# Kernel tuning notes

Measured on AMD Instinct MI355X. Metric: run time of the kernel, lower is better.

## Reference

```python
import jax, jax.numpy as jnp
import numpy as np

N = 50000      # nodes
E = 800000     # edges
IN_DIM = 256
H = 128
OUT_DIM = 64
DEPTH = 3
NEG_SLOPE = 0.2  # DGL GATConv default leaky_relu slope


def setup_inputs() -> dict:
    key = jax.random.key(0)
    ks = jax.random.split(key, 20)
    def nrm(k, shape, fan_in):
        return jax.random.normal(k, shape, jnp.float32) / jnp.sqrt(jnp.float32(fan_in))
    x = jax.random.normal(ks[0], (N, IN_DIM), jnp.float32)
    src = jax.random.randint(ks[1], (E,), 0, N, jnp.int32)
    dst = jax.random.randint(ks[2], (E,), 0, N, jnp.int32)
    # weights stored as [in, out] (y = x @ W + b)
    inp = dict(
        x=x, src=src, dst=dst,
        wx_W=nrm(ks[3], (IN_DIM, H), IN_DIM), wx_b=jnp.zeros((H,), jnp.float32),
        gat_W=nrm(ks[4], (DEPTH, H, H), H), gat_b=jnp.zeros((DEPTH, H), jnp.float32),
        attn_l=nrm(ks[5], (DEPTH, H), H), attn_r=nrm(ks[6], (DEPTH, H), H),
        ig_W=nrm(ks[7], (DEPTH, 2 * H, H), 2 * H), ig_b=jnp.zeros((DEPTH, H), jnp.float32),
        fg_W=nrm(ks[8], (DEPTH, 2 * H, H), 2 * H), fg_b=jnp.zeros((DEPTH, H), jnp.float32),
        og_W=nrm(ks[9], (DEPTH, 2 * H, H), 2 * H), og_b=jnp.zeros((DEPTH, H), jnp.float32),
        st_W=nrm(ks[10], (DEPTH, 2 * H, H), 2 * H), st_b=jnp.zeros((DEPTH, H), jnp.float32),
        out_W=nrm(ks[11], (H, OUT_DIM), H), out_b=jnp.zeros((OUT_DIM,), jnp.float32),
    )
    return inp


def _breadth(h, W, b, a_l, a_r, src, dst):
    """DGL GATConv with 1 head + tanh activation; mean over heads is identity."""
    z = h @ W                                  # [N, H]
    el = z @ a_l                               # [N]
    er = z @ a_r                               # [N]
    e = jax.nn.leaky_relu(el[src] + er[dst], NEG_SLOPE)   # [E]
    # edge softmax over incoming edges of each dst node
    emax = jax.ops.segment_max(e, dst, num_segments=N)    # [N]
    emax = jnp.where(jnp.isfinite(emax), emax, 0.0)       # guard isolated nodes
    ex = jnp.exp(e - emax[dst])                            # [E]
    denom = jax.ops.segment_sum(ex, dst, num_segments=N)   # [N]
    alpha = ex / jnp.maximum(denom, 1e-16)[dst]             # [E]
    agg = jax.ops.segment_sum(alpha[:, None] * z[src], dst, num_segments=N)  # [N, H]
    return jnp.tanh(agg + b)


def reference(x, src, dst, wx_W, wx_b, gat_W, gat_b, attn_l, attn_r,
              ig_W, ig_b, fg_W, fg_b, og_W, og_b, st_W, st_b, out_W, out_b):
    h0 = x @ wx_W + wx_b                       # [N, H]
    h = h0
    collector = []
    for i in range(DEPTH):
        h = _breadth(h, gat_W[i], gat_b[i], attn_l[i], attn_r[i], src, dst)
        collector.append(h)
    mu = h0
    c = jnp.zeros_like(mu)
    for i in range(DEPTH):
        hm = jnp.concatenate([collector[i], mu], axis=1)   # [N, 2H]
        ig = jax.nn.sigmoid(hm @ ig_W[i] + ig_b[i])
        fg = jax.nn.sigmoid(hm @ fg_W[i] + fg_b[i])
        og = jax.nn.sigmoid(hm @ og_W[i] + og_b[i])
        c_tilde = jnp.tanh(hm @ st_W[i] + st_b[i])
        c = fg * c + ig * c_tilde
        mu = og * jnp.tanh(c)
    return jax.nn.relu(mu @ out_W + out_b)     # [N, OUT_DIM]
```

## Files before the change

kernel.cpp:

```cpp
#include <hip/hip_runtime.h>
#include <math.h>
#include <type_traits>

#define NN 50000
#define EE 800000
#define IN_D 256
#define HH 128
#define OUT_D 64
#define DEPTH 3
#define BK 512
#define NBK 98

typedef unsigned short u16;
typedef __bf16  bf16x8 __attribute__((ext_vector_type(8)));
typedef short   short8 __attribute__((ext_vector_type(8)));
typedef float   f32x4  __attribute__((ext_vector_type(4)));

__device__ __forceinline__ u16 f2b(float f){
    unsigned u = __float_as_uint(f);
    u += 0x7fff + ((u>>16)&1);
    return (u16)(u>>16);
}
__device__ __forceinline__ float b2f(u16 h){ return __uint_as_float(((unsigned)h)<<16); }

#define LOG2E 1.4426950408889634f
#if __has_builtin(__builtin_amdgcn_exp2f)
__device__ __forceinline__ float fexp2(float x){ return __builtin_amdgcn_exp2f(x); }
#else
__device__ __forceinline__ float fexp2(float x){ return exp2f(x); }
#endif
#if __has_builtin(__builtin_amdgcn_rcpf)
__device__ __forceinline__ float frcp(float x){ return __builtin_amdgcn_rcpf(x); }
#else
__device__ __forceinline__ float frcp(float x){ return 1.f/x; }
#endif
__device__ __forceinline__ float sigm(float x){ return frcp(1.f + fexp2(-x*LOG2E)); }
__device__ __forceinline__ float ftanh(float x){
    float ax = fabsf(x);
    float u = fexp2(ax * (-2.f*LOG2E));
    float r = (1.f - u) * frcp(1.f + u);
    return copysignf(r, x);
}

enum { EPI_BF=0, EPI_RELU=1, EPI_ZEL=2 };

template<int EPI, int WAVES, int CT, int K, typename TA>
__global__ __launch_bounds__(WAVES*64, 4) void rgemm_k(
    const TA* __restrict__ A1,
    const u16* __restrict__ Bp,
    const float* __restrict__ b1, const float* __restrict__ b2,
    void* __restrict__ Out, float* __restrict__ aux1, float* __restrict__ aux2,
    int Nrows)
{
    constexpr int TH = WAVES*64;
    constexpr int KS = K/32;
    constexpr int M  = WAVES*CT*16;
    __shared__ u16 As[64*K];
    __shared__ float elp[(EPI==EPI_ZEL)?64*WAVES:1];
    __shared__ float erp[(EPI==EPI_ZEL)?64*WAVES:1];

    const int tid = threadIdx.x;
    const int rb  = blockIdx.x*64;

    constexpr int CHUNKS = 64*K/(TH*8);
    #pragma unroll
    for (int c = 0; c < CHUNKS; ++c) {
        int cidx = tid + c*TH;
        int row = cidx & 63, kseg = cidx >> 6;
        int grow = rb + row; if (grow >= Nrows) grow = Nrows-1;
        short8 v;
        if constexpr (std::is_same<TA,float>::value) {
            const float* p = (const float*)A1 + (size_t)grow*K + kseg*8;
            float4 x0 = *(const float4*)p;
            float4 x1 = *(const float4*)(p+4);
            v[0]=(short)f2b(x0.x); v[1]=(short)f2b(x0.y); v[2]=(short)f2b(x0.z); v[3]=(short)f2b(x0.w);
            v[4]=(short)f2b(x1.x); v[5]=(short)f2b(x1.y); v[6]=(short)f2b(x1.z); v[7]=(short)f2b(x1.w);
        } else {
            v = *(const short8*)((const u16*)A1 + (size_t)grow*K + kseg*8);
        }
        int byte = ((row>>4)*KS + (kseg>>2))*1024 + ((kseg&3)*16 + (row&15))*16;
        *(short8*)((char*)As + byte) = v;
    }
    __syncthreads();

    const int lane = tid & 63, w = tid >> 6;
    const int ml = lane & 15, ksel = lane >> 4;
    f32x4 acc[4][CT] = {};
    #pragma unroll
    for (int ks = 0; ks < KS; ++ks) {
        bf16x8 a[4];
        #pragma unroll
        for (int rt = 0; rt < 4; ++rt)
            a[rt] = *(const bf16x8*)((const char*)As + (rt*KS + ks)*1024 + lane*16);
        #pragma unroll
        for (int j = 0; j < CT; ++j) {
            int ctg = j*WAVES + w;
            bf16x8 b = *(const bf16x8*)(Bp + (((size_t)(ctg*KS + ks))<<9) + lane*8);
            #pragma unroll
            for (int rt = 0; rt < 4; ++rt)
                acc[rt][j] = __builtin_amdgcn_mfma_f32_16x16x32_bf16(a[rt], b, acc[rt][j], 0,0,0);
        }
    }

    if constexpr (EPI==EPI_BF || EPI==EPI_RELU) {
        #pragma unroll
        for (int rt = 0; rt < 4; ++rt)
        #pragma unroll
        for (int r = 0; r < 4; ++r) {
            int row = rb + rt*16 + ksel*4 + r;
            if (row >= Nrows) continue;
            #pragma unroll
            for (int j = 0; j < CT; ++j) {
                int gc = (j*WAVES + w)*16 + ml;
                float vv = acc[rt][j][r] + b1[gc];
                if (EPI==EPI_BF) ((u16*)Out)[(size_t)row*M + gc]   = f2b(vv);
                else             ((float*)Out)[(size_t)row*M + gc] = fmaxf(vv, 0.f);
            }
        }
    } else {
        float pel[4][4] = {}, per[4][4] = {};
        #pragma unroll
        for (int j = 0; j < CT; ++j) {
            int gc = (j*WAVES + w)*16 + ml;
            float alc = b1[gc], arc = b2[gc];
            #pragma unroll
            for (int rt = 0; rt < 4; ++rt)
            #pragma unroll
            for (int r = 0; r < 4; ++r) {
                int row = rb + rt*16 + ksel*4 + r;
                float vv = acc[rt][j][r];
                if (row < Nrows) ((u16*)Out)[(size_t)row*HH + gc] = f2b(vv);
                pel[rt][r] = fmaf(vv, alc, pel[rt][r]);
                per[rt][r] = fmaf(vv, arc, per[rt][r]);
            }
        }
        #pragma unroll
        for (int msk = 1; msk < 16; msk <<= 1)
            #pragma unroll
            for (int rt = 0; rt < 4; ++rt)
            #pragma unroll
            for (int r = 0; r < 4; ++r) {
                pel[rt][r] += __shfl_xor(pel[rt][r], msk);
                per[rt][r] += __shfl_xor(per[rt][r], msk);
            }
        if (ml == 0) {
            #pragma unroll
            for (int rt = 0; rt < 4; ++rt)
            #pragma unroll
            for (int r = 0; r < 4; ++r) {
                int lr = rt*16 + ksel*4 + r;
                elp[lr*WAVES + w] = pel[rt][r];
                erp[lr*WAVES + w] = per[rt][r];
            }
        }
        __syncthreads();
        if (tid < 64) {
            int row = rb + tid;
            if (row < Nrows) {
                float s1 = 0.f, s2 = 0.f;
                #pragma unroll
                for (int wv = 0; wv < WAVES; ++wv) { s1 += elp[tid*WAVES+wv]; s2 += erp[tid*WAVES+wv]; }
                aux1[row] = s1; aux2[row] = s2;
            }
        }
    }
}

__global__ __launch_bounds__(512, 3) void depth_k(
    const u16* __restrict__ coll0, const u16* __restrict__ coll1, const u16* __restrict__ coll2,
    const u16* __restrict__ mu0,
    const u16* __restrict__ gateP, const u16* __restrict__ outP,
    const float* __restrict__ igb, const float* __restrict__ stb,
    const float* __restrict__ fgb, const float* __restrict__ ogb,
    const float* __restrict__ outb, float* __restrict__ Out,
    int Nrows)
{
    __shared__ u16 As[64*HH];
    __shared__ u16 Ms[64*HH];
    const int tid = threadIdx.x;
    const int rb  = blockIdx.x*64;
    const int lane = tid & 63, w = tid >> 6;
    const int ml = lane & 15, ksel = lane >> 4;
    const int gcg = w*16 + ml;

    const int c0 = tid, c1 = tid + 512;
    const int row0 = c0 & 63, kg0 = c0 >> 6;
    const int row1 = c1 & 63, kg1 = c1 >> 6;
    int gr0 = rb + row0; if (gr0 >= Nrows) gr0 = Nrows-1;
    int gr1 = rb + row1; if (gr1 >= Nrows) gr1 = Nrows-1;
    const size_t off0 = (size_t)gr0*HH + kg0*8, off1 = (size_t)gr1*HH + kg1*8;
    const int dst0 = ((row0>>4)*4 + (kg0>>2))*1024 + ((kg0&3)*16 + (row0&15))*16;
    const int dst1 = ((row1>>4)*4 + (kg1>>2))*1024 + ((kg1&3)*16 + (row1&15))*16;

    *(short8*)((char*)Ms + dst0) = *(const short8*)(mu0 + off0);
    *(short8*)((char*)Ms + dst1) = *(const short8*)(mu0 + off1);
    short8 pf0 = *(const short8*)(coll0 + off0);
    short8 pf1 = *(const short8*)(coll0 + off1);

    float cc[4][4];
    #pragma unroll
    for (int i = 0; i < DEPTH; ++i) {
        __syncthreads();
        *(short8*)((char*)As + dst0) = pf0;
        *(short8*)((char*)As + dst1) = pf1;
        if (i == 0) { pf0 = *(const short8*)(coll1 + off0); pf1 = *(const short8*)(coll1 + off1); }
        if (i == 1) { pf0 = *(const short8*)(coll2 + off0); pf1 = *(const short8*)(coll2 + off1); }
        __syncthreads();

        f32x4 acc[4][4] = {};
        bf16x8 bc[4];
        #pragma unroll
        for (int g = 0; g < 4; ++g)
            bc[g] = *(const bf16x8*)(gateP + (size_t)i*131072 + (g*8 + w)*4096 + lane*8);
        #pragma unroll
        for (int ks = 0; ks < 8; ++ks) {
            bf16x8 bn[4];
            if (ks < 7) {
                #pragma unroll
                for (int g = 0; g < 4; ++g)
                    bn[g] = *(const bf16x8*)(gateP + (size_t)i*131072 + (g*8 + w)*4096 + (ks+1)*512 + lane*8);
            }
            const char* Sb = (ks < 4) ? (const char*)As : (const char*)Ms;
            bf16x8 a[4];
            #pragma unroll
            for (int rt = 0; rt < 4; ++rt)
                a[rt] = *(const bf16x8*)(Sb + (rt*4 + (ks&3))*1024 + lane*16);
            #pragma unroll
            for (int g = 0; g < 4; ++g)
                #pragma unroll
                for (int rt = 0; rt < 4; ++rt)
                    acc[rt][g] = __builtin_amdgcn_mfma_f32_16x16x32_bf16(a[rt], bc[g], acc[rt][g], 0,0,0);
            if (ks < 7) {
                #pragma unroll
                for (int g = 0; g < 4; ++g) bc[g] = bn[g];
            }
        }
        __syncthreads();

        float bi = igb[i*HH + gcg], bs = stb[i*HH + gcg];
        float bf_ = fgb[i*HH + gcg], bo = ogb[i*HH + gcg];
        const int fks  = gcg >> 5;
        const int shi  = (gcg >> 3) & 3;
        const int elem = gcg & 7;
        #pragma unroll
        for (int rt = 0; rt < 4; ++rt)
        #pragma unroll
        for (int r = 0; r < 4; ++r) {
            float ig = sigm (acc[rt][0][r] + bi);
            float st = ftanh(acc[rt][1][r] + bs);
            float fg = sigm (acc[rt][2][r] + bf_);
            float og = sigm (acc[rt][3][r] + bo);
            float P  = ig * st;
            float cn = (i == 0) ? P : fmaf(fg, cc[rt][r], P);
            cc[rt][r] = cn;
            float mun = og * ftanh(cn);
            int byte = (rt*4 + fks)*1024 + (shi*16 + (ksel*4 + r))*16 + elem*2;
            *(u16*)((char*)Ms + byte) = f2b(mun);
        }
    }
    __syncthreads();

    {
        const int ct = w & 3;
        const int rh = (w >> 2) * 2;
        f32x4 acc[2] = {};
        #pragma unroll
        for (int ks = 0; ks < 4; ++ks) {
            bf16x8 a[2];
            #pragma unroll
            for (int q = 0; q < 2; ++q)
                a[q] = *(const bf16x8*)((const char*)Ms + ((rh+q)*4 + ks)*1024 + lane*16);
            bf16x8 b = *(const bf16x8*)(outP + (size_t)((ct*4 + ks)<<9) + lane*8);
            #pragma unroll
            for (int q = 0; q < 2; ++q)
                acc[q] = __builtin_amdgcn_mfma_f32_16x16x32_bf16(a[q], b, acc[q], 0,0,0);
        }
        int gc = ct*16 + ml;
        float bb = outb[gc];
        #pragma unroll
        for (int q = 0; q < 2; ++q)
        #pragma unroll
        for (int r = 0; r < 4; ++r) {
            int row = rb + (rh + q)*16 + ksel*4 + r;
            if (row < Nrows)
                Out[(size_t)row*OUT_D + gc] = fmaxf(acc[q][r] + bb, 0.f);
        }
    }
}

struct PK  { const float* s; u16* d; int K; int Mc; };
struct PKs { PK t[17]; };
__global__ __launch_bounds__(256) void pack_k(PKs ps){
    const PK t = ps.t[blockIdx.y];
    int o = blockIdx.x*256 + threadIdx.x;
    if (o >= t.K * t.Mc) return;
    int i = o & 7, lane = (o>>3) & 63, rst = o >> 9;
    int KS = t.K >> 5;
    int ks = rst % KS, ct = rst / KS;
    int col = ct*16 + (lane & 15);
    int k   = ks*32 + (lane>>4)*8 + i;
    t.d[o] = f2b(t.s[(size_t)k*t.Mc + col]);
}

__global__ __launch_bounds__(256) void binh_k(const int* __restrict__ dst, int* __restrict__ bcnt){
    __shared__ int h[NBK];
    int t = threadIdx.x;
    if (t < NBK) h[t] = 0;
    __syncthreads();
    int base = blockIdx.x*4096;
    #pragma unroll
    for (int c = 0; c < 16; ++c){ int e = base + c*256 + t; if (e < EE) atomicAdd(&h[dst[e]>>9], 1); }
    __syncthreads();
    if (t < NBK && h[t]) atomicAdd(&bcnt[t], h[t]);
}
__global__ __launch_bounds__(128) void bscan_k(const int* __restrict__ bcnt,
                                               int* __restrict__ bbase, int* __restrict__ gcur){
    __shared__ int s[128];
    int t = threadIdx.x;
    int v = (t < NBK) ? bcnt[t] : 0;
    s[t] = v; __syncthreads();
    for (int off=1; off<128; off<<=1){ int x = (t>=off)? s[t-off] : 0; __syncthreads(); s[t] += x; __syncthreads(); }
    if (t < NBK){ bbase[t] = s[t]-v; gcur[t] = s[t]-v; }
}
__global__ __launch_bounds__(256) void binsc_k(const int* __restrict__ dst, const int* __restrict__ src,
                                               int* __restrict__ gcur, unsigned* __restrict__ staged){
    __shared__ int h[NBK], bb[NBK], lc[NBK];
    int t = threadIdx.x;
    if (t < NBK){ h[t]=0; lc[t]=0; }
    __syncthreads();
    int base = blockIdx.x*4096;
    int d[16], s[16];
    #pragma unroll
    for (int c = 0; c < 16; ++c){
        int e = base + c*256 + t; d[c] = -1;
        if (e < EE){ d[c] = dst[e]; s[c] = src[e]; atomicAdd(&h[d[c]>>9], 1); }
    }
    __syncthreads();
    if (t < NBK && h[t]) bb[t] = atomicAdd(&gcur[t], h[t]);
    __syncthreads();
    #pragma unroll
    for (int c = 0; c < 16; ++c) if (d[c] >= 0){
        int b = d[c]>>9;
        int r = atomicAdd(&lc[b], 1);
        staged[bb[b] + r] = ((unsigned)(d[c] & 511) << 16) | (unsigned)s[c];
    }
}
__global__ __launch_bounds__(BK) void build_k(const int* __restrict__ bcnt, const int* __restrict__ bbase,
                                              const unsigned* __restrict__ staged,
                                              int* __restrict__ rp, int* __restrict__ deg, u16* __restrict__ srcs){
    __shared__ int soff[BK], cur[BK];
    int t = threadIdx.x, bk = blockIdx.x;
    int n0 = bk*BK;
    soff[t] = 0; cur[t] = 0;
    __syncthreads();
    int cb = bcnt[bk], eb = bbase[bk];
    for (int j = t; j < cb; j += BK) atomicAdd(&soff[staged[eb+j]>>16], 1);
    __syncthreads();
    int d0 = soff[t];
    for (int off=1; off<BK; off<<=1){ int x = (t>=off)? soff[t-off] : 0; __syncthreads(); soff[t] += x; __syncthreads(); }
    int ex = soff[t] - d0;
    __syncthreads();
    soff[t] = ex;
    int n = n0 + t;
    if (n < NN){ deg[n] = d0; rp[n] = eb + ex; }
    __syncthreads();
    for (int j = t; j < cb; j += BK){
        unsigned p = staged[eb+j];
        int l = p >> 16;
        int r = atomicAdd(&cur[l], 1);
        srcs[eb + soff[l] + r] = (u16)(p & 0xffff);
    }
}

__global__ __launch_bounds__(256) void gat_k(
    const u16* __restrict__ z, const float* __restrict__ el, const float* __restrict__ er,
    const u16* __restrict__ srcs, const int* __restrict__ rp, const int* __restrict__ deg,
    const float* __restrict__ bias, u16* __restrict__ hout)
{
    int n = blockIdx.x*4 + (threadIdx.x>>6);
    if (n >= NN) return;
    int lane = threadIdx.x & 63;
    int start = rp[n], cnt = deg[n];
    float ern = er[n];
    const int slot = lane >> 4;
    const int ch   = (lane & 15) * 8;
    float acc[8] = {};

    if (cnt <= 64) {
        float v = -1e30f; int s_reg = 0;
        if (lane < cnt) {
            s_reg = srcs[start + lane];
            float tv = el[s_reg] + ern;
            v = tv >= 0.f ? tv : 0.2f*tv;
        }
        float m = v;
        #pragma unroll
        for (int off=1; off<64; off<<=1) m = fmaxf(m, __shfl_xor(m, off));
        float a = (lane < cnt) ? fexp2((v - m)*LOG2E) : 0.f;
        float ss = a;
        #pragma unroll
        for (int off=1; off<64; off<<=1) ss += __shfl_xor(ss, off);
        float a_reg = a * frcp(fmaxf(ss, 1e-16f));

        const int cntp = (cnt + 15) & ~15;
        for (int i = slot; i < cntp; i += 16) {
            float w0 = __shfl(a_reg, i),    w1 = __shfl(a_reg, i+4);
            float w2 = __shfl(a_reg, i+8),  w3 = __shfl(a_reg, i+12);
            int   s0 = __shfl(s_reg, i),    s1 = __shfl(s_reg, i+4);
            int   s2 = __shfl(s_reg, i+8),  s3 = __shfl(s_reg, i+12);
            short8 v0 = *(const short8*)(z + (size_t)s0*HH + ch);
            short8 v1 = *(const short8*)(z + (size_t)s1*HH + ch);
            short8 v2 = *(const short8*)(z + (size_t)s2*HH + ch);
            short8 v3 = *(const short8*)(z + (size_t)s3*HH + ch);
            #pragma unroll
            for (int j=0;j<8;j++)
                acc[j] = fmaf(w3, b2f((u16)v3[j]),
                         fmaf(w2, b2f((u16)v2[j]),
                         fmaf(w1, b2f((u16)v1[j]),
                         fmaf(w0, b2f((u16)v0[j]), acc[j]))));
        }
    } else {
        float m = -1e30f;
        for (int i=lane; i<cnt; i+=64){ float tv = el[srcs[start+i]] + ern; tv = tv>=0.f?tv:0.2f*tv; m = fmaxf(m, tv); }
        #pragma unroll
        for (int off=1; off<64; off<<=1) m = fmaxf(m, __shfl_xor(m, off));
        float ss = 0.f;
        for (int i=lane; i<cnt; i+=64){ float tv = el[srcs[start+i]] + ern; tv = tv>=0.f?tv:0.2f*tv; ss += fexp2((tv-m)*LOG2E); }
        #pragma unroll
        for (int off=1; off<64; off<<=1) ss += __shfl_xor(ss, off);
        float inv = frcp(fmaxf(ss, 1e-16f));
        for (int i=slot; i<cnt; i+=4) {
            int sn = srcs[start+i];
            float tv = el[sn] + ern; tv = tv>=0.f?tv:0.2f*tv;
            float w0 = fexp2((tv-m)*LOG2E) * inv;
            short8 v0 = *(const short8*)(z + (size_t)sn*HH + ch);
            #pragma unroll
            for (int j=0;j<8;j++) acc[j] = fmaf(w0, b2f((u16)v0[j]), acc[j]);
        }
    }
    #pragma unroll
    for (int j=0;j<8;j++){ acc[j] += __shfl_xor(acc[j],16); acc[j] += __shfl_xor(acc[j],32); }
    if (slot == 0) {
        short8 o8;
        #pragma unroll
        for (int j=0;j<8;j++) o8[j] = (short)f2b(ftanh(acc[j] + bias[ch+j]));
        *(short8*)(hout + (size_t)n*HH + ch) = o8;
    }
}

extern "C" void kernel_launch(void* const* d_in, const int* in_sizes, int n_in,
                              void* d_out, int out_size, void* d_ws, size_t ws_size,
                              hipStream_t stream)
{
    const float* x    = (const float*)d_in[0];
    const int*   src  = (const int*)d_in[1];
    const int*   dst  = (const int*)d_in[2];
    const float* wxW  = (const float*)d_in[3];
    const float* wxb  = (const float*)d_in[4];
    const float* gatW = (const float*)d_in[5];
    const float* gatb = (const float*)d_in[6];
    const float* attl = (const float*)d_in[7];
    const float* attr = (const float*)d_in[8];
    const float* igW  = (const float*)d_in[9];
    const float* igb  = (const float*)d_in[10];
    const float* fgW  = (const float*)d_in[11];
    const float* fgb  = (const float*)d_in[12];
    const float* ogW  = (const float*)d_in[13];
    const float* ogb  = (const float*)d_in[14];
    const float* stW  = (const float*)d_in[15];
    const float* stb  = (const float*)d_in[16];
    const float* outW = (const float*)d_in[17];
    const float* outb = (const float*)d_in[18];

    char* w = (char*)d_ws;
    auto alloc = [&](size_t bytes)->char* { char* p = w; w += (bytes + 255) & ~(size_t)255; return p; };
    const size_t NH = (size_t)NN * HH;
    u16*      muB    = (u16*)alloc(NH*2);
    u16*      zB     = (u16*)alloc(NH*2);
    u16*      coll0  = (u16*)alloc(NH*2);
    u16*      coll1  = (u16*)alloc(NH*2);
    u16*      coll2  = (u16*)alloc(NH*2);
    float*    el     = (float*)alloc((size_t)NN*4);
    float*    er     = (float*)alloc((size_t)NN*4);
    unsigned* staged = (unsigned*)alloc((size_t)EE*4);
    u16*      srcs   = (u16*)alloc((size_t)EE*2);
    int*      deg    = (int*)alloc((size_t)NN*4);
    int*      rp     = (int*)alloc((size_t)NN*4);
    int*      bcnt   = (int*)alloc(128*4);
    int*      bbase  = (int*)alloc(128*4);
    int*      gcur   = (int*)alloc(128*4);
    u16*      bpool  = (u16*)alloc(483328*2);
    u16* wxP   = bpool;
    u16* gatP  = bpool + 32768;
    u16* gateP = bpool + 81920;
    u16* outP  = bpool + 475136;
    u16* coll[3] = {coll0, coll1, coll2};

    PKs ps;
    ps.t[0] = {wxW, wxP, IN_D, HH};
    for (int i=0;i<3;i++) ps.t[1+i]  = {gatW + (size_t)i*HH*HH,   gatP  + i*16384,           HH,   HH};
    for (int i=0;i<3;i++) ps.t[4+i]  = {igW  + (size_t)i*2*HH*HH, gateP + i*131072,          2*HH, HH};
    for (int i=0;i<3;i++) ps.t[7+i]  = {stW  + (size_t)i*2*HH*HH, gateP + i*131072 + 32768,  2*HH, HH};
    for (int i=0;i<3;i++) ps.t[10+i] = {fgW  + (size_t)i*2*HH*HH, gateP + i*131072 + 65536,  2*HH, HH};
    for (int i=0;i<3;i++) ps.t[13+i] = {ogW  + (size_t)i*2*HH*HH, gateP + i*131072 + 98304,  2*HH, HH};
    ps.t[16] = {outW, outP, HH, OUT_D};
    pack_k<<<dim3(128,17), 256, 0, stream>>>(ps);

    hipMemsetAsync(bcnt, 0, 128*4, stream);
    const int gE = (EE + 4095) / 4096;
    binh_k <<<gE, 256, 0, stream>>>(dst, bcnt);
    bscan_k<<<1, 128, 0, stream>>>(bcnt, bbase, gcur);
    binsc_k<<<gE, 256, 0, stream>>>(dst, src, gcur, staged);
    build_k<<<NBK, BK, 0, stream>>>(bcnt, bbase, staged, rp, deg, srcs);

    const int gN = (NN + 63) / 64;
    const int gA = (NN + 3) / 4;

    rgemm_k<EPI_BF,4,2,IN_D,float><<<gN, 256, 0, stream>>>(
        x, wxP, wxb, nullptr, muB, nullptr, nullptr, NN);

    const u16* hin = muB;
    for (int i = 0; i < DEPTH; ++i) {
        rgemm_k<EPI_ZEL,4,2,HH,u16><<<gN, 256, 0, stream>>>(
            hin, gatP + i*16384, attl + i*HH, attr + i*HH, zB, el, er, NN);
        gat_k<<<gA, 256, 0, stream>>>(zB, el, er, srcs, rp, deg, gatb + i*HH, coll[i]);
        hin = coll[i];
    }

    depth_k<<<gN, 512, 0, stream>>>(coll0, coll1, coll2, muB, gateP, outP,
                                    igb, stb, fgb, ogb, outb, (float*)d_out, NN);
}
```

Measured before the change: 303.1 us.

## Shrink depth kernel tiles to 32 rows with 4 waves per block

The fused LSTM-gate depth kernel now processes 32 rows per 256-thread block instead of 64 rows per 512-thread block. Each wave covers 32 output columns across all four gates, and the register double-buffering of B fragments is dropped in favor of direct loads per MFMA group. The goal is to double the number of blocks and cut LDS use per block for better occupancy and load balance. The cost is that each gate weight fragment is reused across only two row tiles instead of four, which raises global/L2 weight traffic per row.

```diff
diff --git a/kernel.cpp b/kernel.cpp
--- a/kernel.cpp
+++ b/kernel.cpp
@@ -166,7 +166,7 @@
     }
 }
 
-__global__ __launch_bounds__(512, 3) void depth_k(
+__global__ __launch_bounds__(256, 4) void depth_k(
     const u16* __restrict__ coll0, const u16* __restrict__ coll1, const u16* __restrict__ coll2,
     const u16* __restrict__ mu0,
     const u16* __restrict__ gateP, const u16* __restrict__ outP,
@@ -175,17 +175,16 @@
     const float* __restrict__ outb, float* __restrict__ Out,
     int Nrows)
 {
-    __shared__ u16 As[64*HH];
-    __shared__ u16 Ms[64*HH];
+    __shared__ u16 As[32*HH];
+    __shared__ u16 Ms[32*HH];
     const int tid = threadIdx.x;
-    const int rb  = blockIdx.x*64;
+    const int rb  = blockIdx.x*32;
     const int lane = tid & 63, w = tid >> 6;
     const int ml = lane & 15, ksel = lane >> 4;
-    const int gcg = w*16 + ml;
-
-    const int c0 = tid, c1 = tid + 512;
-    const int row0 = c0 & 63, kg0 = c0 >> 6;
-    const int row1 = c1 & 63, kg1 = c1 >> 6;
+
+    const int c0 = tid, c1 = tid + 256;
+    const int row0 = c0 & 31, kg0 = c0 >> 5;
+    const int row1 = c1 & 31, kg1 = c1 >> 5;
     int gr0 = rb + row0; if (gr0 >= Nrows) gr0 = Nrows-1;
     int gr1 = rb + row1; if (gr1 >= Nrows) gr1 = Nrows-1;
     const size_t off0 = (size_t)gr0*HH + kg0*8, off1 = (size_t)gr1*HH + kg1*8;
@@ -197,7 +196,7 @@
     short8 pf0 = *(const short8*)(coll0 + off0);
     short8 pf1 = *(const short8*)(coll0 + off1);
 
-    float cc[4][4];
+    float cc[2][2][4];
     #pragma unroll
     for (int i = 0; i < DEPTH; ++i) {
         __syncthreads();
@@ -207,83 +206,74 @@
         if (i == 1) { pf0 = *(const short8*)(coll2 + off0); pf1 = *(const short8*)(coll2 + off1); }
         __syncthreads();
 
-        f32x4 acc[4][4] = {};
-        bf16x8 bc[4];
-        #pragma unroll
-        for (int g = 0; g < 4; ++g)
-            bc[g] = *(const bf16x8*)(gateP + (size_t)i*131072 + (g*8 + w)*4096 + lane*8);
+        f32x4 acc[2][4][2] = {};
         #pragma unroll
         for (int ks = 0; ks < 8; ++ks) {
-            bf16x8 bn[4];
-            if (ks < 7) {
+            const char* Sb = (ks < 4) ? (const char*)As : (const char*)Ms;
+            bf16x8 a[2];
+            #pragma unroll
+            for (int rt = 0; rt < 2; ++rt)
+                a[rt] = *(const bf16x8*)(Sb + (rt*4 + (ks&3))*1024 + lane*16);
+            #pragma unroll
+            for (int g = 0; g < 4; ++g)
+            #pragma unroll
+            for (int j = 0; j < 2; ++j) {
+                bf16x8 b = *(const bf16x8*)(gateP + (size_t)i*131072 + ((g*8 + w*2 + j)*8 + ks)*512 + lane*8);
                 #pragma unroll
-                for (int g = 0; g < 4; ++g)
-                    bn[g] = *(const bf16x8*)(gateP + (size_t)i*131072 + (g*8 + w)*4096 + (ks+1)*512 + lane*8);
-            }
-            const char* Sb = (ks < 4) ? (const char*)As : (const char*)Ms;
-            bf16x8 a[4];
-            #pragma unroll
-            for (int rt = 0; rt < 4; ++rt)
-                a[rt] = *(const bf16x8*)(Sb + (rt*4 + (ks&3))*1024 + lane*16);
-            #pragma unroll
-            for (int g = 0; g < 4; ++g)
-                #pragma unroll
-                for (int rt = 0; rt < 4; ++rt)
-                    acc[rt][g] = __builtin_amdgcn_mfma_f32_16x16x32_bf16(a[rt], bc[g], acc[rt][g], 0,0,0);
-            if (ks < 7) {
-                #pragma unroll
-                for (int g = 0; g < 4; ++g) bc[g] = bn[g];
+                for (int rt = 0; rt < 2; ++rt)
+                    acc[rt][g][j] = __builtin_amdgcn_mfma_f32_16x16x32_bf16(a[rt], b, acc[rt][g][j], 0,0,0);
             }
         }
         __syncthreads();
 
-        float bi = igb[i*HH + gcg], bs = stb[i*HH + gcg];
-        float bf_ = fgb[i*HH + gcg], bo = ogb[i*HH + gcg];
-        const int fks  = gcg >> 5;
-        const int shi  = (gcg >> 3) & 3;
-        const int elem = gcg & 7;
-        #pragma unroll
-        for (int rt = 0; rt < 4; ++rt)
-        #pragma unroll
-        for (int r = 0; r < 4; ++r) {
-            float ig = sigm (acc[rt][0][r] + bi);
-            float st = ftanh(acc[rt][1][r] + bs);
-            float fg = sigm (acc[rt][2][r] + bf_);
-            float og = sigm (acc[rt][3][r] + bo);
-            float P  = ig * st;
-            float cn = (i == 0) ? P : fmaf(fg, cc[rt][r], P);
-            cc[rt][r] = cn;
-            float mun = og * ftanh(cn);
-            int byte = (rt*4 + fks)*1024 + (shi*16 + (ksel*4 + r))*16 + elem*2;
-            *(u16*)((char*)Ms + byte) = f2b(mun);
+        #pragma unroll
+        for (int j = 0; j < 2; ++j) {
+            int col = w*32 + j*16 + ml;
+            float bi = igb[i*HH + col], bs = stb[i*HH + col];
+            float bf_ = fgb[i*HH + col], bo = ogb[i*HH + col];
+            const int slothi = (j*2 + (ml>>3))*16;
+            const int elem   = ml & 7;
+            #pragma unroll
+            for (int rt = 0; rt < 2; ++rt)
+            #pragma unroll
+            for (int r = 0; r < 4; ++r) {
+                float ig = sigm (acc[rt][0][j][r] + bi);
+                float st = ftanh(acc[rt][1][j][r] + bs);
+                float fg = sigm (acc[rt][2][j][r] + bf_);
+                float og = sigm (acc[rt][3][j][r] + bo);
+                float P  = ig * st;
+                float cn = (i == 0) ? P : fmaf(fg, cc[rt][j][r], P);
+                cc[rt][j][r] = cn;
+                float mun = og * ftanh(cn);
+                int byte = (rt*4 + w)*1024 + (slothi + ksel*4 + r)*16 + elem*2;
+                *(u16*)((char*)Ms + byte) = f2b(mun);
+            }
         }
     }
     __syncthreads();
 
     {
-        const int ct = w & 3;
-        const int rh = (w >> 2) * 2;
         f32x4 acc[2] = {};
         #pragma unroll
         for (int ks = 0; ks < 4; ++ks) {
             bf16x8 a[2];
             #pragma unroll
-            for (int q = 0; q < 2; ++q)
-                a[q] = *(const bf16x8*)((const char*)Ms + ((rh+q)*4 + ks)*1024 + lane*16);
-            bf16x8 b = *(const bf16x8*)(outP + (size_t)((ct*4 + ks)<<9) + lane*8);
-            #pragma unroll
-            for (int q = 0; q < 2; ++q)
-                acc[q] = __builtin_amdgcn_mfma_f32_16x16x32_bf16(a[q], b, acc[q], 0,0,0);
-        }
-        int gc = ct*16 + ml;
+            for (int rt = 0; rt < 2; ++rt)
+                a[rt] = *(const bf16x8*)((const char*)Ms + (rt*4 + ks)*1024 + lane*16);
+            bf16x8 b = *(const bf16x8*)(outP + (size_t)((w*4 + ks)<<9) + lane*8);
+            #pragma unroll
+            for (int rt = 0; rt < 2; ++rt)
+                acc[rt] = __builtin_amdgcn_mfma_f32_16x16x32_bf16(a[rt], b, acc[rt], 0,0,0);
+        }
+        int gc = w*16 + ml;
         float bb = outb[gc];
         #pragma unroll
-        for (int q = 0; q < 2; ++q)
+        for (int rt = 0; rt < 2; ++rt)
         #pragma unroll
         for (int r = 0; r < 4; ++r) {
-            int row = rb + (rh + q)*16 + ksel*4 + r;
+            int row = rb + rt*16 + ksel*4 + r;
             if (row < Nrows)
-                Out[(size_t)row*OUT_D + gc] = fmaxf(acc[q][r] + bb, 0.f);
+                Out[(size_t)row*OUT_D + gc] = fmaxf(acc[rt][r] + bb, 0.f);
         }
     }
 }
@@ -513,8 +503,9 @@
     binsc_k<<<gE, 256, 0, stream>>>(dst, src, gcur, staged);
     build_k<<<NBK, BK, 0, stream>>>(bcnt, bbase, staged, rp, deg, srcs);
 
-    const int gN = (NN + 63) / 64;
-    const int gA = (NN + 3) / 4;
+    const int gN  = (NN + 63) / 64;
+    const int gN2 = (NN + 31) / 32;
+    const int gA  = (NN + 3) / 4;
 
     rgemm_k<EPI_BF,4,2,IN_D,float><<<gN, 256, 0, stream>>>(
         x, wxP, wxb, nullptr, muB, nullptr, nullptr, NN);
@@ -527,6 +518,6 @@
         hin = coll[i];
     }
 
-    depth_k<<<gN, 512, 0, stream>>>(coll0, coll1, coll2, muB, gateP, outP,
-                                    igb, stb, fgb, ogb, outb, (float*)d_out, NN);
-}
+    depth_k<<<gN2, 256, 0, stream>>>(coll0, coll1, coll2, muB, gateP, outP,
+                                     igb, stb, fgb, ogb, outb, (float*)d_out, NN);
+}
```

Result: slower. 342.7 us (+13.0%).
